# Optimization experiments

Hardware: AMD Instinct MI355X
Metric: run time of the kernel (lower is better)

## Reference

```python
import jax, jax.numpy as jnp
import numpy as np
from jax import lax

LN_EPS = 1e-5

def _expert_ffn_all(x, w1, b1, g_ln, b_ln, w2, b2):
    # x: [B,S,D]; w1: [E,D,F]; w2: [E,F,O]
    h = jnp.einsum('bsd,edf->bsef', x, w1) + b1[None, None]          # [B,S,E,F]
    h = jax.nn.gelu(h, approximate=False)                            # torch default GELU (erf)
    mu = jnp.mean(h, axis=-1, keepdims=True)
    var = jnp.var(h, axis=-1, keepdims=True)
    h = (h - mu) / jnp.sqrt(var + LN_EPS) * g_ln[None, None] + b_ln[None, None]
    return jnp.einsum('bsef,efo->bseo', h, w2) + b2[None, None]      # [B,S,E,O]

def _moe_forward(x, w_gate, w1, b1, g_ln, b_ln, w2, b2):
    B, S, D = x.shape
    E = w_gate.shape[1]
    k = max(1, S // E)  # capacity_factor=1.0
    logits = jnp.einsum('bsd,de->bse', x, w_gate)                    # x_gated [B,S,E]
    probs = jax.nn.softmax(logits, axis=-1)
    # expert-choice top-k along the sequence dim of the raw logits
    _, idx = lax.top_k(jnp.transpose(logits, (0, 2, 1)), k)          # [B,E,k]
    b_ix = jnp.arange(B)[:, None, None]
    e_ix = jnp.arange(E)[None, :, None]
    mask_t = jnp.zeros((B, E, S), dtype=probs.dtype).at[b_ix, e_ix, idx].set(1.0)
    gate_scores = probs * jnp.transpose(mask_t, (0, 2, 1))           # [B,S,E]
    expert_out = _expert_ffn_all(x, w1, b1, g_ln, b_ln, w2, b2)      # [B,S,E,O]
    moe_output = jnp.einsum('bse,bseo->bso', gate_scores, expert_out)
    return moe_output, logits

def setup_inputs() -> dict:
    key = jax.random.key(0)
    ks = jax.random.split(key, 4)
    B, S, D, F, O, E = 2, 2048, 1024, 2048, 1024, 8
    sc1 = 1.0 / np.sqrt(D)
    sc2 = 1.0 / np.sqrt(F)
    return {
        'x': jax.random.normal(ks[0], (B, S, D), jnp.float32),
        'w_gate': jax.random.normal(ks[1], (D, E), jnp.float32) * sc1,
        'w1': jax.random.normal(ks[2], (E, D, F), jnp.float32) * sc1,
        'b1': jnp.zeros((E, F), jnp.float32),
        'g_ln': jnp.ones((E, F), jnp.float32),
        'b_ln': jnp.zeros((E, F), jnp.float32),
        'w2': jax.random.normal(ks[3], (E, F, O), jnp.float32) * sc2,
        'b2': jnp.zeros((E, O), jnp.float32),
    }

def reference(x, w_gate, w1, b1, g_ln, b_ln, w2, b2):
    return _moe_forward(x, w_gate, w1, b1, g_ln, b_ln, w2, b2)
```

## Files before the change

kernel.cpp:

```cpp
#include <hip/hip_runtime.h>
#include <cstdint>
#include <cstddef>

typedef __attribute__((ext_vector_type(8))) short bf16x8;
typedef __attribute__((ext_vector_type(4))) float f32x4;

#define S_    2048
#define D_    1024
#define F_    2048
#define O_    1024
#define E_    8
#define KCAP  256
#define ROWS  512
#define NTOK  4096

#define BM 64
#define BN 64
#define BK 64
#define TILE_ELEMS (BM * BK)

__device__ __forceinline__ unsigned short f2bf(float f) {
  unsigned int u = __float_as_uint(f);
  u = (u + 0x7fffu + ((u >> 16) & 1u)) >> 16;
  return (unsigned short)u;
}
__device__ __forceinline__ float bf2f(unsigned short h) {
  return __uint_as_float(((unsigned int)h) << 16);
}

__device__ __forceinline__ void gload16(void* lds, const void* g) {
  auto gp = (__attribute__((address_space(1))) unsigned int*)(uintptr_t)g;
  auto lp = (__attribute__((address_space(3))) unsigned int*)(unsigned int)(uintptr_t)lds;
  __builtin_amdgcn_global_load_lds(gp, lp, 16, 0, 0);
}

__global__ void gating_kernel(const float* __restrict__ x, const float* __restrict__ wg,
                              float* __restrict__ logits, float* __restrict__ probs,
                              unsigned short* __restrict__ xb) {
  const int wave = threadIdx.x >> 6, lane = threadIdx.x & 63;
  const int t = blockIdx.x * 4 + wave;
  const float* xr = x + (size_t)t * D_;
  double acc[8] = {0, 0, 0, 0, 0, 0, 0, 0};
  const int d0 = lane * 16;
#pragma unroll
  for (int i = 0; i < 4; i++) {
    float4 xv = *(const float4*)&xr[d0 + i * 4];
    union { ushort4 u4; unsigned short u[4]; } cv;
    cv.u[0] = f2bf(xv.x); cv.u[1] = f2bf(xv.y); cv.u[2] = f2bf(xv.z); cv.u[3] = f2bf(xv.w);
    *(ushort4*)&xb[(size_t)t * D_ + d0 + i * 4] = cv.u4;
    float xs[4] = {xv.x, xv.y, xv.z, xv.w};
#pragma unroll
    for (int j = 0; j < 4; j++) {
      const float4* wr = (const float4*)&wg[(size_t)(d0 + i * 4 + j) * 8];
      float4 w0 = wr[0], w1v = wr[1];
      double xd = (double)xs[j];
      acc[0] += xd * (double)w0.x;  acc[1] += xd * (double)w0.y;
      acc[2] += xd * (double)w0.z;  acc[3] += xd * (double)w0.w;
      acc[4] += xd * (double)w1v.x; acc[5] += xd * (double)w1v.y;
      acc[6] += xd * (double)w1v.z; acc[7] += xd * (double)w1v.w;
    }
  }
#pragma unroll
  for (int off = 32; off; off >>= 1) {
#pragma unroll
    for (int e = 0; e < 8; e++) acc[e] += __shfl_down(acc[e], off);
  }
  if (lane == 0) {
    double m = acc[0];
    for (int e = 1; e < 8; e++) m = acc[e] > m ? acc[e] : m;
    double p[8]; double s = 0;
    for (int e = 0; e < 8; e++) { p[e] = exp(acc[e] - m); s += p[e]; }
    const double inv = 1.0 / s;
    for (int e = 0; e < 8; e++) {
      logits[(size_t)t * 8 + e] = (float)acc[e];
      probs [(size_t)t * 8 + e] = (float)(p[e] * inv);
    }
  }
}

__global__ void transpose_cvt_kernel(const float* __restrict__ in, unsigned short* __restrict__ out,
                                     const int R, const int C) {
  __shared__ float t[64][65];
  const int e = blockIdx.z;
  const float* inp = in + (size_t)e * R * C;
  unsigned short* outp = out + (size_t)e * R * C;
  const int r0 = blockIdx.y * 64, c0 = blockIdx.x * 64;
  const int tid = threadIdx.x;
  const int lr = tid >> 4;
  const int lc = (tid & 15) * 4;
#pragma unroll
  for (int i = 0; i < 4; i++) {
    const int r = lr + i * 16;
    const float4 v = *(const float4*)&inp[(size_t)(r0 + r) * C + c0 + lc];
    t[r][lc] = v.x; t[r][lc + 1] = v.y; t[r][lc + 2] = v.z; t[r][lc + 3] = v.w;
  }
  __syncthreads();
#pragma unroll
  for (int i = 0; i < 4; i++) {
    const int oc = lr + i * 16;
    union { ushort4 u4; unsigned short u[4]; } u;
#pragma unroll
    for (int j = 0; j < 4; j++) u.u[j] = f2bf(t[lc + j][oc]);
    *(ushort4*)&outp[(size_t)(c0 + oc) * R + r0 + lc] = u.u4;
  }
}

__global__ void topk_kernel(const float* __restrict__ logits, const float* __restrict__ probs,
                            int* __restrict__ sel, float* __restrict__ gate) {
  __shared__ unsigned int keys[S_];
  const int idx = blockIdx.x;
  const int seg = idx & 7;
  const int be = idx >> 3;
  const int b = be >> 3;
  const int e = be & 7;
  const int tid = threadIdx.x;
  for (int i = tid; i < S_; i += 256) {
    unsigned int u = __float_as_uint(logits[((size_t)(b * S_ + i)) * E_ + e]);
    keys[i] = u ^ ((u & 0x80000000u) ? 0xFFFFFFFFu : 0x80000000u);
  }
  __syncthreads();
  const int s = seg * 256 + tid;
  const unsigned int vk = keys[s];
  const int wave = tid >> 6;
  const int W0 = seg * 256 + wave * 64;
  int rank = 0;
#pragma unroll 4
  for (int i = 0; i < W0; i += 4) {
    const uint4 kv = *(const uint4*)&keys[i];
    rank += (kv.x >= vk) + (kv.y >= vk) + (kv.z >= vk) + (kv.w >= vk);
  }
#pragma unroll
  for (int j = 0; j < 64; j++) {
    const int i = W0 + j;
    const unsigned int kv = keys[i];
    rank += (kv > vk) || (kv == vk && i < s);
  }
#pragma unroll 4
  for (int i = W0 + 64; i < S_; i += 4) {
    const uint4 kv = *(const uint4*)&keys[i];
    rank += (kv.x > vk) + (kv.y > vk) + (kv.z > vk) + (kv.w > vk);
  }
  if (rank < KCAP) {
    sel [e * ROWS + b * KCAP + rank] = b * S_ + s;
    gate[e * ROWS + b * KCAP + rank] = probs[((size_t)(b * S_ + s)) * E_ + e];
  }
}

__global__ __launch_bounds__(256, 4) void gemm1_kernel(
    const unsigned short* __restrict__ xb,
    const unsigned short* __restrict__ w1t,
    const float* __restrict__ b1,
    const int* __restrict__ sel,
    unsigned short* __restrict__ hbuf) {
  __shared__ unsigned short As[2 * TILE_ELEMS];
  __shared__ unsigned short Bs[2 * TILE_ELEMS];
  const int bid = blockIdx.x;
  const int lid = (bid & 7) * 256 + (bid >> 3);
  const int e   = lid >> 8;
  const int rem = lid & 255;
  const int n0  = (rem >> 3) * BN;
  const int m0  = (rem & 7) * BM;
  const int tid = threadIdx.x;
  const int wave = tid >> 6, lane = tid & 63;
  const int wr = wave >> 1, wc = wave & 1;

  const int srow = lane >> 3;
  const int schunk = (lane & 7) ^ srow;
  const unsigned short* asrc[2];
  const unsigned short* bsrc[2];
#pragma unroll
  for (int j = 0; j < 2; j++) {
    const int r = wave * 16 + j * 8 + srow;
    const int tok = sel[e * ROWS + m0 + r];
    asrc[j] = xb + (size_t)tok * D_ + schunk * 8;
    bsrc[j] = w1t + ((size_t)e * F_ + n0 + r) * D_ + schunk * 8;
  }

  f32x4 acc[2][2];
#pragma unroll
  for (int mi = 0; mi < 2; mi++)
#pragma unroll
    for (int nj = 0; nj < 2; nj++) acc[mi][nj] = (f32x4){0.f, 0.f, 0.f, 0.f};

  const int fr = lane & 15;

  auto stage = [&](int buf, int k0) {
#pragma unroll
    for (int j = 0; j < 2; j++) {
      gload16(&As[buf * TILE_ELEMS + (wave * 16 + j * 8) * BK], asrc[j] + k0);
      gload16(&Bs[buf * TILE_ELEMS + (wave * 16 + j * 8) * BK], bsrc[j] + k0);
    }
  };
  auto compute = [&](int buf) {
    const unsigned short* Ab = &As[buf * TILE_ELEMS];
    const unsigned short* Bb = &Bs[buf * TILE_ELEMS];
    bf16x8 a[2][2], b[2][2];
#pragma unroll
    for (int kk = 0; kk < 2; kk++) {
      const int xch = ((kk * 4 + (lane >> 4)) ^ (lane & 7)) * 8;
#pragma unroll
      for (int mi = 0; mi < 2; mi++)
        a[kk][mi] = *(const bf16x8*)&Ab[(wr * 32 + mi * 16 + fr) * BK + xch];
#pragma unroll
      for (int nj = 0; nj < 2; nj++)
        b[kk][nj] = *(const bf16x8*)&Bb[(wc * 32 + nj * 16 + fr) * BK + xch];
    }
#pragma unroll
    for (int kk = 0; kk < 2; kk++)
#pragma unroll
      for (int mi = 0; mi < 2; mi++)
#pragma unroll
        for (int nj = 0; nj < 2; nj++)
          acc[mi][nj] = __builtin_amdgcn_mfma_f32_16x16x32_bf16(a[kk][mi], b[kk][nj], acc[mi][nj], 0, 0, 0);
  };

  stage(0, 0);
  __syncthreads();
  int cur = 0;
  for (int t = 0; t < D_ / BK - 1; t++) {
    stage(cur ^ 1, (t + 1) * BK);
    compute(cur);
    __syncthreads();
    cur ^= 1;
  }
  compute(cur);

  const int lr = (lane >> 4) * 4;
#pragma unroll
  for (int mi = 0; mi < 2; mi++)
#pragma unroll
    for (int nj = 0; nj < 2; nj++)
#pragma unroll
      for (int rg = 0; rg < 4; rg++) {
        const int row = m0 + wr * 32 + mi * 16 + lr + rg;
        const int col = n0 + wc * 32 + nj * 16 + fr;
        float v = acc[mi][nj][rg] + b1[e * F_ + col];
        v = 0.5f * v * (1.0f + erff(v * 0.70710678118654752f));
        hbuf[((size_t)e * ROWS + row) * F_ + col] = f2bf(v);
      }
}

__global__ void ln_kernel(unsigned short* __restrict__ hbuf,
                          const float* __restrict__ g_ln, const float* __restrict__ b_ln) {
  const int row = blockIdx.x;
  const int e = row >> 9;
  unsigned short* hr = hbuf + (size_t)row * F_;
  const int tid = threadIdx.x;
  union { bf16x8 v; unsigned short u[8]; } u;
  u.v = *(const bf16x8*)&hr[tid * 8];
  float vals[8]; float s1 = 0.f, s2 = 0.f;
#pragma unroll
  for (int j = 0; j < 8; j++) { float f = bf2f(u.u[j]); vals[j] = f; s1 += f; s2 += f * f; }
#pragma unroll
  for (int off = 32; off; off >>= 1) { s1 += __shfl_down(s1, off); s2 += __shfl_down(s2, off); }
  __shared__ float rs[8];
  const int wave = tid >> 6, lane = tid & 63;
  if (lane == 0) { rs[wave] = s1; rs[wave + 4] = s2; }
  __syncthreads();
  const float t1 = rs[0] + rs[1] + rs[2] + rs[3];
  const float t2 = rs[4] + rs[5] + rs[6] + rs[7];
  const float mu = t1 * (1.f / F_);
  const float var = t2 * (1.f / F_) - mu * mu;
  const float rstd = rsqrtf(var + 1e-5f);
  const float4* gl4 = (const float4*)(g_ln + (size_t)e * F_ + tid * 8);
  const float4* bl4 = (const float4*)(b_ln + (size_t)e * F_ + tid * 8);
  float4 g0 = gl4[0], g1 = gl4[1], bb0 = bl4[0], bb1 = bl4[1];
  float gs[8] = {g0.x, g0.y, g0.z, g0.w, g1.x, g1.y, g1.z, g1.w};
  float bs[8] = {bb0.x, bb0.y, bb0.z, bb0.w, bb1.x, bb1.y, bb1.z, bb1.w};
  union { bf16x8 v; unsigned short u[8]; } o;
#pragma unroll
  for (int j = 0; j < 8; j++)
    o.u[j] = f2bf((vals[j] - mu) * rstd * gs[j] + bs[j]);
  *(bf16x8*)&hr[tid * 8] = o.v;
}

__global__ __launch_bounds__(256, 4) void gemm2_kernel(
    const unsigned short* __restrict__ hbuf,
    const unsigned short* __restrict__ w2t,
    const float* __restrict__ b2,
    const int* __restrict__ sel, const float* __restrict__ gate,
    float* __restrict__ out) {
  __shared__ unsigned short As[2 * TILE_ELEMS];
  __shared__ unsigned short Bs[2 * TILE_ELEMS];
  const int bid = blockIdx.x;
  const int lid = (bid & 7) * 128 + (bid >> 3);
  const int e   = lid >> 7;
  const int rem = lid & 127;
  const int n0  = (rem >> 3) * BN;
  const int m0  = (rem & 7) * BM;
  const int tid = threadIdx.x;
  const int wave = tid >> 6, lane = tid & 63;
  const int wr = wave >> 1, wc = wave & 1;

  const int srow = lane >> 3;
  const int schunk = (lane & 7) ^ srow;
  const unsigned short* asrc[2];
  const unsigned short* bsrc[2];
#pragma unroll
  for (int j = 0; j < 2; j++) {
    const int r = wave * 16 + j * 8 + srow;
    asrc[j] = hbuf + ((size_t)e * ROWS + m0 + r) * F_ + schunk * 8;
    bsrc[j] = w2t + ((size_t)e * O_ + n0 + r) * F_ + schunk * 8;
  }

  f32x4 acc[2][2];
#pragma unroll
  for (int mi = 0; mi < 2; mi++)
#pragma unroll
    for (int nj = 0; nj < 2; nj++) acc[mi][nj] = (f32x4){0.f, 0.f, 0.f, 0.f};

  const int fr = lane & 15;

  auto stage = [&](int buf, int k0) {
#pragma unroll
    for (int j = 0; j < 2; j++) {
      gload16(&As[buf * TILE_ELEMS + (wave * 16 + j * 8) * BK], asrc[j] + k0);
      gload16(&Bs[buf * TILE_ELEMS + (wave * 16 + j * 8) * BK], bsrc[j] + k0);
    }
  };
  auto compute = [&](int buf) {
    const unsigned short* Ab = &As[buf * TILE_ELEMS];
    const unsigned short* Bb = &Bs[buf * TILE_ELEMS];
    bf16x8 a[2][2], b[2][2];
#pragma unroll
    for (int kk = 0; kk < 2; kk++) {
      const int xch = ((kk * 4 + (lane >> 4)) ^ (lane & 7)) * 8;
#pragma unroll
      for (int mi = 0; mi < 2; mi++)
        a[kk][mi] = *(const bf16x8*)&Ab[(wr * 32 + mi * 16 + fr) * BK + xch];
#pragma unroll
      for (int nj = 0; nj < 2; nj++)
        b[kk][nj] = *(const bf16x8*)&Bb[(wc * 32 + nj * 16 + fr) * BK + xch];
    }
#pragma unroll
    for (int kk = 0; kk < 2; kk++)
#pragma unroll
      for (int mi = 0; mi < 2; mi++)
#pragma unroll
        for (int nj = 0; nj < 2; nj++)
          acc[mi][nj] = __builtin_amdgcn_mfma_f32_16x16x32_bf16(a[kk][mi], b[kk][nj], acc[mi][nj], 0, 0, 0);
  };

  stage(0, 0);
  __syncthreads();
  int cur = 0;
  for (int t = 0; t < F_ / BK - 1; t++) {
    stage(cur ^ 1, (t + 1) * BK);
    compute(cur);
    __syncthreads();
    cur ^= 1;
  }
  compute(cur);

  const int lr = (lane >> 4) * 4;
#pragma unroll
  for (int mi = 0; mi < 2; mi++) {
#pragma unroll
    for (int rg = 0; rg < 4; rg++) {
      const int row = m0 + wr * 32 + mi * 16 + lr + rg;
      const int tok = sel[e * ROWS + row];
      const float g = gate[e * ROWS + row];
#pragma unroll
      for (int nj = 0; nj < 2; nj++) {
        const int col = n0 + wc * 32 + nj * 16 + fr;
        const float v = acc[mi][nj][rg] + b2[e * O_ + col];
        atomicAdd(&out[(size_t)tok * O_ + col], g * v);
      }
    }
  }
}

extern "C" void kernel_launch(void* const* d_in, const int* in_sizes, int n_in,
                              void* d_out, int out_size, void* d_ws, size_t ws_size,
                              hipStream_t stream) {
  const float* x     = (const float*)d_in[0];
  const float* wg    = (const float*)d_in[1];
  const float* w1    = (const float*)d_in[2];
  const float* b1    = (const float*)d_in[3];
  const float* g_ln  = (const float*)d_in[4];
  const float* b_ln  = (const float*)d_in[5];
  const float* w2    = (const float*)d_in[6];
  const float* b2    = (const float*)d_in[7];
  float* out = (float*)d_out;
  float* out_logits = out + (size_t)NTOK * O_;

  char* wsb = (char*)d_ws;
  unsigned short* xb   = (unsigned short*)(wsb + 0);
  unsigned short* w1t  = (unsigned short*)(wsb + 8388608);
  unsigned short* w2t  = (unsigned short*)(wsb + 41943040);
  unsigned short* hbuf = (unsigned short*)(wsb + 75497472);
  float* probs = (float*)(wsb + 92274688);
  int*   sel   = (int*)  (wsb + 92405760);
  float* gate  = (float*)(wsb + 92422144);

  hipMemsetAsync(d_out, 0, (size_t)NTOK * O_ * sizeof(float), stream);

  gating_kernel<<<NTOK / 4, 256, 0, stream>>>(x, wg, out_logits, probs, xb);
  transpose_cvt_kernel<<<dim3(F_ / 64, D_ / 64, E_), 256, 0, stream>>>(w1, w1t, D_, F_);
  transpose_cvt_kernel<<<dim3(O_ / 64, F_ / 64, E_), 256, 0, stream>>>(w2, w2t, F_, O_);
  topk_kernel<<<2 * E_ * 8, 256, 0, stream>>>(out_logits, probs, sel, gate);
  gemm1_kernel<<<(F_ / BN) * (ROWS / BM) * E_, 256, 0, stream>>>(xb, w1t, b1, sel, hbuf);
  ln_kernel<<<E_ * ROWS, 256, 0, stream>>>(hbuf, g_ln, b_ln);
  gemm2_kernel<<<(O_ / BN) * (ROWS / BM) * E_, 256, 0, stream>>>(hbuf, w2t, b2, sel, gate, out);
}
```

Measured before the change: 156.6 us.

## Enlarge GEMM tiles to 128x128 with 8 waves and split-K in gemm2

Both expert GEMMs move from 64x64 tiles with 4 waves to 128x128 tiles with 8 waves, where each wave computes a 64x32 sub-tile. This raises arithmetic intensity per LDS load and cuts redundant global traffic. The pipeline now prefetches two stages ahead using explicit vmcnt waits and raw s_barrier in place of __syncthreads. gemm2 also splits K in half to keep 512 blocks, which doubles the atomic adds into the output and adds the bias only from the first half.

```diff
diff --git a/kernel.cpp b/kernel.cpp
--- a/kernel.cpp
+++ b/kernel.cpp
@@ -14,10 +14,7 @@
 #define ROWS  512
 #define NTOK  4096
 
-#define BM 64
-#define BN 64
 #define BK 64
-#define TILE_ELEMS (BM * BK)
 
 __device__ __forceinline__ unsigned short f2bf(float f) {
   unsigned int u = __float_as_uint(f);
@@ -146,94 +143,95 @@
   }
 }
 
-__global__ __launch_bounds__(256, 4) void gemm1_kernel(
+__global__ __launch_bounds__(512, 4) void gemm1_kernel(
     const unsigned short* __restrict__ xb,
     const unsigned short* __restrict__ w1t,
     const float* __restrict__ b1,
     const int* __restrict__ sel,
     unsigned short* __restrict__ hbuf) {
-  __shared__ unsigned short As[2 * TILE_ELEMS];
-  __shared__ unsigned short Bs[2 * TILE_ELEMS];
+  __shared__ unsigned short As[2][128 * 64];
+  __shared__ unsigned short Bs[2][128 * 64];
   const int bid = blockIdx.x;
-  const int lid = (bid & 7) * 256 + (bid >> 3);
-  const int e   = lid >> 8;
-  const int rem = lid & 255;
-  const int n0  = (rem >> 3) * BN;
-  const int m0  = (rem & 7) * BM;
+  const int lid = (bid & 7) * 64 + (bid >> 3);
+  const int e   = lid >> 6;
+  const int rem = lid & 63;
+  const int m0  = (rem & 3) * 128;
+  const int n0  = (rem >> 2) * 128;
   const int tid = threadIdx.x;
   const int wave = tid >> 6, lane = tid & 63;
-  const int wr = wave >> 1, wc = wave & 1;
-
-  const int srow = lane >> 3;
-  const int schunk = (lane & 7) ^ srow;
-  const unsigned short* asrc[2];
-  const unsigned short* bsrc[2];
-#pragma unroll
-  for (int j = 0; j < 2; j++) {
-    const int r = wave * 16 + j * 8 + srow;
-    const int tok = sel[e * ROWS + m0 + r];
-    asrc[j] = xb + (size_t)tok * D_ + schunk * 8;
-    bsrc[j] = w1t + ((size_t)e * F_ + n0 + r) * D_ + schunk * 8;
-  }
-
-  f32x4 acc[2][2];
-#pragma unroll
-  for (int mi = 0; mi < 2; mi++)
+  const int wrow = wave >> 2;
+  const int wcol = wave & 3;
+
+  const int srow = tid >> 3;
+  const int schunk = ((tid & 7) ^ (srow & 7)) * 8;
+  const unsigned short* a0 = xb + (size_t)sel[e * ROWS + m0 + srow] * D_ + schunk;
+  const unsigned short* a1 = xb + (size_t)sel[e * ROWS + m0 + srow + 64] * D_ + schunk;
+  const unsigned short* b0 = w1t + ((size_t)e * F_ + n0 + srow) * D_ + schunk;
+  const unsigned short* b1p = w1t + ((size_t)e * F_ + n0 + srow + 64) * D_ + schunk;
+  const int ldst0 = wave * 512;
+  const int ldst1 = 4096 + wave * 512;
+
+  f32x4 acc[4][2];
+#pragma unroll
+  for (int mi = 0; mi < 4; mi++)
 #pragma unroll
     for (int nj = 0; nj < 2; nj++) acc[mi][nj] = (f32x4){0.f, 0.f, 0.f, 0.f};
 
+  auto stage = [&](int buf, int t) {
+    const int k0 = t * BK;
+    gload16(&As[buf][ldst0], a0 + k0);
+    gload16(&As[buf][ldst1], a1 + k0);
+    gload16(&Bs[buf][ldst0], b0 + k0);
+    gload16(&Bs[buf][ldst1], b1p + k0);
+  };
   const int fr = lane & 15;
-
-  auto stage = [&](int buf, int k0) {
-#pragma unroll
-    for (int j = 0; j < 2; j++) {
-      gload16(&As[buf * TILE_ELEMS + (wave * 16 + j * 8) * BK], asrc[j] + k0);
-      gload16(&Bs[buf * TILE_ELEMS + (wave * 16 + j * 8) * BK], bsrc[j] + k0);
+  auto compute = [&](int buf) {
+    const unsigned short* Ab = As[buf];
+    const unsigned short* Bb = Bs[buf];
+#pragma unroll
+    for (int kk = 0; kk < 2; kk++) {
+      const int q = kk * 4 + (lane >> 4);
+      bf16x8 a[4], b[2];
+#pragma unroll
+      for (int mi = 0; mi < 4; mi++) {
+        const int r = wrow * 64 + mi * 16 + fr;
+        a[mi] = *(const bf16x8*)&Ab[r * 64 + ((q ^ (r & 7)) * 8)];
+      }
+#pragma unroll
+      for (int nj = 0; nj < 2; nj++) {
+        const int r = wcol * 32 + nj * 16 + fr;
+        b[nj] = *(const bf16x8*)&Bb[r * 64 + ((q ^ (r & 7)) * 8)];
+      }
+#pragma unroll
+      for (int mi = 0; mi < 4; mi++)
+#pragma unroll
+        for (int nj = 0; nj < 2; nj++)
+          acc[mi][nj] = __builtin_amdgcn_mfma_f32_16x16x32_bf16(a[mi], b[nj], acc[mi][nj], 0, 0, 0);
     }
   };
-  auto compute = [&](int buf) {
-    const unsigned short* Ab = &As[buf * TILE_ELEMS];
-    const unsigned short* Bb = &Bs[buf * TILE_ELEMS];
-    bf16x8 a[2][2], b[2][2];
-#pragma unroll
-    for (int kk = 0; kk < 2; kk++) {
-      const int xch = ((kk * 4 + (lane >> 4)) ^ (lane & 7)) * 8;
-#pragma unroll
-      for (int mi = 0; mi < 2; mi++)
-        a[kk][mi] = *(const bf16x8*)&Ab[(wr * 32 + mi * 16 + fr) * BK + xch];
-#pragma unroll
-      for (int nj = 0; nj < 2; nj++)
-        b[kk][nj] = *(const bf16x8*)&Bb[(wc * 32 + nj * 16 + fr) * BK + xch];
-    }
-#pragma unroll
-    for (int kk = 0; kk < 2; kk++)
-#pragma unroll
-      for (int mi = 0; mi < 2; mi++)
-#pragma unroll
-        for (int nj = 0; nj < 2; nj++)
-          acc[mi][nj] = __builtin_amdgcn_mfma_f32_16x16x32_bf16(a[kk][mi], b[kk][nj], acc[mi][nj], 0, 0, 0);
-  };
-
+
+  const int NT = D_ / BK;
   stage(0, 0);
-  __syncthreads();
-  int cur = 0;
-  for (int t = 0; t < D_ / BK - 1; t++) {
-    stage(cur ^ 1, (t + 1) * BK);
-    compute(cur);
-    __syncthreads();
-    cur ^= 1;
-  }
-  compute(cur);
-
-  const int lr = (lane >> 4) * 4;
-#pragma unroll
-  for (int mi = 0; mi < 2; mi++)
+  stage(1, 1);
+  for (int t = 0; t < NT; t++) {
+    if (t < NT - 1) asm volatile("s_waitcnt vmcnt(4)" ::: "memory");
+    else            asm volatile("s_waitcnt vmcnt(0)" ::: "memory");
+    asm volatile("s_barrier" ::: "memory");
+    compute(t & 1);
+    if (t + 2 < NT) {
+      asm volatile("s_barrier" ::: "memory");
+      stage(t & 1, t + 2);
+    }
+  }
+
+#pragma unroll
+  for (int mi = 0; mi < 4; mi++)
 #pragma unroll
     for (int nj = 0; nj < 2; nj++)
 #pragma unroll
       for (int rg = 0; rg < 4; rg++) {
-        const int row = m0 + wr * 32 + mi * 16 + lr + rg;
-        const int col = n0 + wc * 32 + nj * 16 + fr;
+        const int row = m0 + wrow * 64 + mi * 16 + (lane >> 4) * 4 + rg;
+        const int col = n0 + wcol * 32 + nj * 16 + fr;
         float v = acc[mi][nj][rg] + b1[e * F_ + col];
         v = 0.5f * v * (1.0f + erff(v * 0.70710678118654752f));
         hbuf[((size_t)e * ROWS + row) * F_ + col] = f2bf(v);
@@ -274,96 +272,101 @@
   *(bf16x8*)&hr[tid * 8] = o.v;
 }
 
-__global__ __launch_bounds__(256, 4) void gemm2_kernel(
+__global__ __launch_bounds__(512, 4) void gemm2_kernel(
     const unsigned short* __restrict__ hbuf,
     const unsigned short* __restrict__ w2t,
     const float* __restrict__ b2,
     const int* __restrict__ sel, const float* __restrict__ gate,
     float* __restrict__ out) {
-  __shared__ unsigned short As[2 * TILE_ELEMS];
-  __shared__ unsigned short Bs[2 * TILE_ELEMS];
+  __shared__ unsigned short As[2][128 * 64];
+  __shared__ unsigned short Bs[2][128 * 64];
   const int bid = blockIdx.x;
-  const int lid = (bid & 7) * 128 + (bid >> 3);
-  const int e   = lid >> 7;
-  const int rem = lid & 127;
-  const int n0  = (rem >> 3) * BN;
-  const int m0  = (rem & 7) * BM;
+  const int lid = (bid & 7) * 64 + (bid >> 3);
+  const int e   = lid >> 6;
+  const int rem = lid & 63;
+  const int khalf = rem & 1;
+  const int m0  = ((rem >> 1) & 3) * 128;
+  const int n0  = (rem >> 3) * 128;
+  const int koff = khalf * (F_ / 2);
   const int tid = threadIdx.x;
   const int wave = tid >> 6, lane = tid & 63;
-  const int wr = wave >> 1, wc = wave & 1;
-
-  const int srow = lane >> 3;
-  const int schunk = (lane & 7) ^ srow;
-  const unsigned short* asrc[2];
-  const unsigned short* bsrc[2];
-#pragma unroll
-  for (int j = 0; j < 2; j++) {
-    const int r = wave * 16 + j * 8 + srow;
-    asrc[j] = hbuf + ((size_t)e * ROWS + m0 + r) * F_ + schunk * 8;
-    bsrc[j] = w2t + ((size_t)e * O_ + n0 + r) * F_ + schunk * 8;
-  }
-
-  f32x4 acc[2][2];
-#pragma unroll
-  for (int mi = 0; mi < 2; mi++)
+  const int wrow = wave >> 2;
+  const int wcol = wave & 3;
+
+  const int srow = tid >> 3;
+  const int schunk = ((tid & 7) ^ (srow & 7)) * 8;
+  const unsigned short* a0 = hbuf + ((size_t)e * ROWS + m0 + srow) * F_ + koff + schunk;
+  const unsigned short* a1 = hbuf + ((size_t)e * ROWS + m0 + srow + 64) * F_ + koff + schunk;
+  const unsigned short* b0 = w2t + ((size_t)e * O_ + n0 + srow) * F_ + koff + schunk;
+  const unsigned short* b1p = w2t + ((size_t)e * O_ + n0 + srow + 64) * F_ + koff + schunk;
+  const int ldst0 = wave * 512;
+  const int ldst1 = 4096 + wave * 512;
+
+  f32x4 acc[4][2];
+#pragma unroll
+  for (int mi = 0; mi < 4; mi++)
 #pragma unroll
     for (int nj = 0; nj < 2; nj++) acc[mi][nj] = (f32x4){0.f, 0.f, 0.f, 0.f};
 
+  auto stage = [&](int buf, int t) {
+    const int k0 = t * BK;
+    gload16(&As[buf][ldst0], a0 + k0);
+    gload16(&As[buf][ldst1], a1 + k0);
+    gload16(&Bs[buf][ldst0], b0 + k0);
+    gload16(&Bs[buf][ldst1], b1p + k0);
+  };
   const int fr = lane & 15;
-
-  auto stage = [&](int buf, int k0) {
-#pragma unroll
-    for (int j = 0; j < 2; j++) {
-      gload16(&As[buf * TILE_ELEMS + (wave * 16 + j * 8) * BK], asrc[j] + k0);
-      gload16(&Bs[buf * TILE_ELEMS + (wave * 16 + j * 8) * BK], bsrc[j] + k0);
+  auto compute = [&](int buf) {
+    const unsigned short* Ab = As[buf];
+    const unsigned short* Bb = Bs[buf];
+#pragma unroll
+    for (int kk = 0; kk < 2; kk++) {
+      const int q = kk * 4 + (lane >> 4);
+      bf16x8 a[4], b[2];
+#pragma unroll
+      for (int mi = 0; mi < 4; mi++) {
+        const int r = wrow * 64 + mi * 16 + fr;
+        a[mi] = *(const bf16x8*)&Ab[r * 64 + ((q ^ (r & 7)) * 8)];
+      }
+#pragma unroll
+      for (int nj = 0; nj < 2; nj++) {
+        const int r = wcol * 32 + nj * 16 + fr;
+        b[nj] = *(const bf16x8*)&Bb[r * 64 + ((q ^ (r & 7)) * 8)];
+      }
+#pragma unroll
+      for (int mi = 0; mi < 4; mi++)
+#pragma unroll
+        for (int nj = 0; nj < 2; nj++)
+          acc[mi][nj] = __builtin_amdgcn_mfma_f32_16x16x32_bf16(a[mi], b[nj], acc[mi][nj], 0, 0, 0);
     }
   };
-  auto compute = [&](int buf) {
-    const unsigned short* Ab = &As[buf * TILE_ELEMS];
-    const unsigned short* Bb = &Bs[buf * TILE_ELEMS];
-    bf16x8 a[2][2], b[2][2];
-#pragma unroll
-    for (int kk = 0; kk < 2; kk++) {
-      const int xch = ((kk * 4 + (lane >> 4)) ^ (lane & 7)) * 8;
-#pragma unroll
-      for (int mi = 0; mi < 2; mi++)
-        a[kk][mi] = *(const bf16x8*)&Ab[(wr * 32 + mi * 16 + fr) * BK + xch];
-#pragma unroll
-      for (int nj = 0; nj < 2; nj++)
-        b[kk][nj] = *(const bf16x8*)&Bb[(wc * 32 + nj * 16 + fr) * BK + xch];
-    }
-#pragma unroll
-    for (int kk = 0; kk < 2; kk++)
-#pragma unroll
-      for (int mi = 0; mi < 2; mi++)
-#pragma unroll
-        for (int nj = 0; nj < 2; nj++)
-          acc[mi][nj] = __builtin_amdgcn_mfma_f32_16x16x32_bf16(a[kk][mi], b[kk][nj], acc[mi][nj], 0, 0, 0);
-  };
-
+
+  const int NT = (F_ / 2) / BK;
   stage(0, 0);
-  __syncthreads();
-  int cur = 0;
-  for (int t = 0; t < F_ / BK - 1; t++) {
-    stage(cur ^ 1, (t + 1) * BK);
-    compute(cur);
-    __syncthreads();
-    cur ^= 1;
-  }
-  compute(cur);
-
-  const int lr = (lane >> 4) * 4;
-#pragma unroll
-  for (int mi = 0; mi < 2; mi++) {
+  stage(1, 1);
+  for (int t = 0; t < NT; t++) {
+    if (t < NT - 1) asm volatile("s_waitcnt vmcnt(4)" ::: "memory");
+    else            asm volatile("s_waitcnt vmcnt(0)" ::: "memory");
+    asm volatile("s_barrier" ::: "memory");
+    compute(t & 1);
+    if (t + 2 < NT) {
+      asm volatile("s_barrier" ::: "memory");
+      stage(t & 1, t + 2);
+    }
+  }
+
+#pragma unroll
+  for (int mi = 0; mi < 4; mi++) {
 #pragma unroll
     for (int rg = 0; rg < 4; rg++) {
-      const int row = m0 + wr * 32 + mi * 16 + lr + rg;
+      const int row = m0 + wrow * 64 + mi * 16 + (lane >> 4) * 4 + rg;
       const int tok = sel[e * ROWS + row];
       const float g = gate[e * ROWS + row];
 #pragma unroll
       for (int nj = 0; nj < 2; nj++) {
-        const int col = n0 + wc * 32 + nj * 16 + fr;
-        const float v = acc[mi][nj][rg] + b2[e * O_ + col];
+        const int col = n0 + wcol * 32 + nj * 16 + fr;
+        float v = acc[mi][nj][rg];
+        if (khalf == 0) v += b2[e * O_ + col];
         atomicAdd(&out[(size_t)tok * O_ + col], g * v);
       }
     }
@@ -399,7 +402,7 @@
   transpose_cvt_kernel<<<dim3(F_ / 64, D_ / 64, E_), 256, 0, stream>>>(w1, w1t, D_, F_);
   transpose_cvt_kernel<<<dim3(O_ / 64, F_ / 64, E_), 256, 0, stream>>>(w2, w2t, F_, O_);
   topk_kernel<<<2 * E_ * 8, 256, 0, stream>>>(out_logits, probs, sel, gate);
-  gemm1_kernel<<<(F_ / BN) * (ROWS / BM) * E_, 256, 0, stream>>>(xb, w1t, b1, sel, hbuf);
+  gemm1_kernel<<<512, 512, 0, stream>>>(xb, w1t, b1, sel, hbuf);
   ln_kernel<<<E_ * ROWS, 256, 0, stream>>>(hbuf, g_ln, b_ln);
-  gemm2_kernel<<<(O_ / BN) * (ROWS / BM) * E_, 256, 0, stream>>>(hbuf, w2t, b2, sel, gate, out);
-}
+  gemm2_kernel<<<512, 512, 0, stream>>>(hbuf, w2t, b2, sel, gate, out);
+}
```

Measured after the change: 162.7 us. +3.9%, slower.

## Split-K the second GEMM and replace atomic scatter with a per-token combine kernel

Applied to the files above, without the earlier changes.

gemm2 now splits the F reduction into two halves, which doubles the block count, and writes plain partial results to a workspace buffer that reuses the w1t region. A new combine kernel uses a token→row entry map written by topk to sum the gated partials plus bias for each token. This removes the output memset and the float atomics. Both GEMMs also drop LDS double buffering for a single buffer with two barriers per step and raise launch bounds to 8 blocks per CU, which trades load/compute overlap for occupancy.

```diff
diff --git a/kernel.cpp b/kernel.cpp
--- a/kernel.cpp
+++ b/kernel.cpp
@@ -106,7 +106,8 @@
 }
 
 __global__ void topk_kernel(const float* __restrict__ logits, const float* __restrict__ probs,
-                            int* __restrict__ sel, float* __restrict__ gate) {
+                            int* __restrict__ sel, float* __restrict__ gate,
+                            int* __restrict__ entry) {
   __shared__ unsigned int keys[S_];
   const int idx = blockIdx.x;
   const int seg = idx & 7;
@@ -141,19 +142,20 @@
     rank += (kv.x > vk) + (kv.y > vk) + (kv.z > vk) + (kv.w > vk);
   }
   if (rank < KCAP) {
-    sel [e * ROWS + b * KCAP + rank] = b * S_ + s;
-    gate[e * ROWS + b * KCAP + rank] = probs[((size_t)(b * S_ + s)) * E_ + e];
-  }
-}
-
-__global__ __launch_bounds__(256, 4) void gemm1_kernel(
-    const unsigned short* __restrict__ xb,
-    const unsigned short* __restrict__ w1t,
-    const float* __restrict__ b1,
-    const int* __restrict__ sel,
+    const int row = b * KCAP + rank;
+    const int tok = b * S_ + s;
+    sel  [e * ROWS + row] = tok;
+    gate [e * ROWS + row] = probs[(size_t)tok * E_ + e];
+    entry[tok * E_ + e]   = row + 1;
+  }
+}
+
+__global__ __launch_bounds__(256, 8) void gemm1_kernel(
+    const unsigned short* __restrict__ xb, const unsigned short* __restrict__ w1t,
+    const float* __restrict__ b1, const int* __restrict__ sel,
     unsigned short* __restrict__ hbuf) {
-  __shared__ unsigned short As[2 * TILE_ELEMS];
-  __shared__ unsigned short Bs[2 * TILE_ELEMS];
+  __shared__ unsigned short As[TILE_ELEMS];
+  __shared__ unsigned short Bs[TILE_ELEMS];
   const int bid = blockIdx.x;
   const int lid = (bid & 7) * 256 + (bid >> 3);
   const int e   = lid >> 8;
@@ -184,26 +186,24 @@
 
   const int fr = lane & 15;
 
-  auto stage = [&](int buf, int k0) {
+  for (int t = 0; t < D_ / BK; t++) {
+    const int k0 = t * BK;
 #pragma unroll
     for (int j = 0; j < 2; j++) {
-      gload16(&As[buf * TILE_ELEMS + (wave * 16 + j * 8) * BK], asrc[j] + k0);
-      gload16(&Bs[buf * TILE_ELEMS + (wave * 16 + j * 8) * BK], bsrc[j] + k0);
-    }
-  };
-  auto compute = [&](int buf) {
-    const unsigned short* Ab = &As[buf * TILE_ELEMS];
-    const unsigned short* Bb = &Bs[buf * TILE_ELEMS];
+      gload16(&As[(wave * 16 + j * 8) * BK], asrc[j] + k0);
+      gload16(&Bs[(wave * 16 + j * 8) * BK], bsrc[j] + k0);
+    }
+    __syncthreads();
     bf16x8 a[2][2], b[2][2];
 #pragma unroll
     for (int kk = 0; kk < 2; kk++) {
       const int xch = ((kk * 4 + (lane >> 4)) ^ (lane & 7)) * 8;
 #pragma unroll
       for (int mi = 0; mi < 2; mi++)
-        a[kk][mi] = *(const bf16x8*)&Ab[(wr * 32 + mi * 16 + fr) * BK + xch];
+        a[kk][mi] = *(const bf16x8*)&As[(wr * 32 + mi * 16 + fr) * BK + xch];
 #pragma unroll
       for (int nj = 0; nj < 2; nj++)
-        b[kk][nj] = *(const bf16x8*)&Bb[(wc * 32 + nj * 16 + fr) * BK + xch];
+        b[kk][nj] = *(const bf16x8*)&Bs[(wc * 32 + nj * 16 + fr) * BK + xch];
     }
 #pragma unroll
     for (int kk = 0; kk < 2; kk++)
@@ -212,18 +212,8 @@
 #pragma unroll
         for (int nj = 0; nj < 2; nj++)
           acc[mi][nj] = __builtin_amdgcn_mfma_f32_16x16x32_bf16(a[kk][mi], b[kk][nj], acc[mi][nj], 0, 0, 0);
-  };
-
-  stage(0, 0);
-  __syncthreads();
-  int cur = 0;
-  for (int t = 0; t < D_ / BK - 1; t++) {
-    stage(cur ^ 1, (t + 1) * BK);
-    compute(cur);
     __syncthreads();
-    cur ^= 1;
-  }
-  compute(cur);
+  }
 
   const int lr = (lane >> 4) * 4;
 #pragma unroll
@@ -274,20 +264,20 @@
   *(bf16x8*)&hr[tid * 8] = o.v;
 }
 
-__global__ __launch_bounds__(256, 4) void gemm2_kernel(
+__global__ __launch_bounds__(256, 8) void gemm2_partial_kernel(
     const unsigned short* __restrict__ hbuf,
     const unsigned short* __restrict__ w2t,
-    const float* __restrict__ b2,
-    const int* __restrict__ sel, const float* __restrict__ gate,
-    float* __restrict__ out) {
-  __shared__ unsigned short As[2 * TILE_ELEMS];
-  __shared__ unsigned short Bs[2 * TILE_ELEMS];
+    float* __restrict__ part) {
+  __shared__ unsigned short As[TILE_ELEMS];
+  __shared__ unsigned short Bs[TILE_ELEMS];
   const int bid = blockIdx.x;
-  const int lid = (bid & 7) * 128 + (bid >> 3);
-  const int e   = lid >> 7;
-  const int rem = lid & 127;
-  const int n0  = (rem >> 3) * BN;
-  const int m0  = (rem & 7) * BM;
+  const int lid = (bid & 7) * 256 + (bid >> 3);
+  const int e     = lid >> 8;
+  const int rem   = lid & 255;
+  const int khalf = rem & 1;
+  const int m0    = ((rem >> 1) & 7) * BM;
+  const int n0    = (rem >> 4) * BN;
+  const int koff  = khalf * (F_ / 2);
   const int tid = threadIdx.x;
   const int wave = tid >> 6, lane = tid & 63;
   const int wr = wave >> 1, wc = wave & 1;
@@ -299,8 +289,8 @@
 #pragma unroll
   for (int j = 0; j < 2; j++) {
     const int r = wave * 16 + j * 8 + srow;
-    asrc[j] = hbuf + ((size_t)e * ROWS + m0 + r) * F_ + schunk * 8;
-    bsrc[j] = w2t + ((size_t)e * O_ + n0 + r) * F_ + schunk * 8;
+    asrc[j] = hbuf + ((size_t)e * ROWS + m0 + r) * F_ + koff + schunk * 8;
+    bsrc[j] = w2t + ((size_t)e * O_ + n0 + r) * F_ + koff + schunk * 8;
   }
 
   f32x4 acc[2][2];
@@ -311,26 +301,24 @@
 
   const int fr = lane & 15;
 
-  auto stage = [&](int buf, int k0) {
+  for (int t = 0; t < (F_ / 2) / BK; t++) {
+    const int k0 = t * BK;
 #pragma unroll
     for (int j = 0; j < 2; j++) {
-      gload16(&As[buf * TILE_ELEMS + (wave * 16 + j * 8) * BK], asrc[j] + k0);
-      gload16(&Bs[buf * TILE_ELEMS + (wave * 16 + j * 8) * BK], bsrc[j] + k0);
-    }
-  };
-  auto compute = [&](int buf) {
-    const unsigned short* Ab = &As[buf * TILE_ELEMS];
-    const unsigned short* Bb = &Bs[buf * TILE_ELEMS];
+      gload16(&As[(wave * 16 + j * 8) * BK], asrc[j] + k0);
+      gload16(&Bs[(wave * 16 + j * 8) * BK], bsrc[j] + k0);
+    }
+    __syncthreads();
     bf16x8 a[2][2], b[2][2];
 #pragma unroll
     for (int kk = 0; kk < 2; kk++) {
       const int xch = ((kk * 4 + (lane >> 4)) ^ (lane & 7)) * 8;
 #pragma unroll
       for (int mi = 0; mi < 2; mi++)
-        a[kk][mi] = *(const bf16x8*)&Ab[(wr * 32 + mi * 16 + fr) * BK + xch];
+        a[kk][mi] = *(const bf16x8*)&As[(wr * 32 + mi * 16 + fr) * BK + xch];
 #pragma unroll
       for (int nj = 0; nj < 2; nj++)
-        b[kk][nj] = *(const bf16x8*)&Bb[(wc * 32 + nj * 16 + fr) * BK + xch];
+        b[kk][nj] = *(const bf16x8*)&Bs[(wc * 32 + nj * 16 + fr) * BK + xch];
     }
 #pragma unroll
     for (int kk = 0; kk < 2; kk++)
@@ -339,35 +327,46 @@
 #pragma unroll
         for (int nj = 0; nj < 2; nj++)
           acc[mi][nj] = __builtin_amdgcn_mfma_f32_16x16x32_bf16(a[kk][mi], b[kk][nj], acc[mi][nj], 0, 0, 0);
-  };
-
-  stage(0, 0);
-  __syncthreads();
-  int cur = 0;
-  for (int t = 0; t < F_ / BK - 1; t++) {
-    stage(cur ^ 1, (t + 1) * BK);
-    compute(cur);
     __syncthreads();
-    cur ^= 1;
-  }
-  compute(cur);
-
+  }
+
+  float* pbase = part + (size_t)khalf * (E_ * ROWS) * O_;
   const int lr = (lane >> 4) * 4;
 #pragma unroll
-  for (int mi = 0; mi < 2; mi++) {
+  for (int mi = 0; mi < 2; mi++)
 #pragma unroll
     for (int rg = 0; rg < 4; rg++) {
       const int row = m0 + wr * 32 + mi * 16 + lr + rg;
-      const int tok = sel[e * ROWS + row];
-      const float g = gate[e * ROWS + row];
 #pragma unroll
       for (int nj = 0; nj < 2; nj++) {
         const int col = n0 + wc * 32 + nj * 16 + fr;
-        const float v = acc[mi][nj][rg] + b2[e * O_ + col];
-        atomicAdd(&out[(size_t)tok * O_ + col], g * v);
+        pbase[((size_t)(e * ROWS) + row) * O_ + col] = acc[mi][nj][rg];
       }
     }
-  }
+}
+
+__global__ void combine_kernel(const float* __restrict__ part, const int* __restrict__ entry,
+                               const float* __restrict__ gate, const float* __restrict__ b2,
+                               float* __restrict__ out) {
+  const int tok = blockIdx.x;
+  const int c = threadIdx.x * 4;
+  float4 acc = {0.f, 0.f, 0.f, 0.f};
+#pragma unroll
+  for (int e = 0; e < E_; e++) {
+    const int r1 = entry[tok * E_ + e];
+    if (r1) {
+      const int idx = e * ROWS + (r1 - 1);
+      const float g = gate[idx];
+      const float4 p0 = *(const float4*)&part[(size_t)idx * O_ + c];
+      const float4 p1 = *(const float4*)&part[(size_t)(E_ * ROWS + idx) * O_ + c];
+      const float4 bb = *(const float4*)&b2[e * O_ + c];
+      acc.x += g * (p0.x + p1.x + bb.x);
+      acc.y += g * (p0.y + p1.y + bb.y);
+      acc.z += g * (p0.z + p1.z + bb.z);
+      acc.w += g * (p0.w + p1.w + bb.w);
+    }
+  }
+  *(float4*)&out[(size_t)tok * O_ + c] = acc;
 }
 
 extern "C" void kernel_launch(void* const* d_in, const int* in_sizes, int n_in,
@@ -392,14 +391,17 @@
   float* probs = (float*)(wsb + 92274688);
   int*   sel   = (int*)  (wsb + 92405760);
   float* gate  = (float*)(wsb + 92422144);
-
-  hipMemsetAsync(d_out, 0, (size_t)NTOK * O_ * sizeof(float), stream);
+  int*   entry = (int*)  (wsb + 92438528);
+  float* part  = (float*)(wsb + 8388608);
+
+  hipMemsetAsync(entry, 0, (size_t)NTOK * E_ * sizeof(int), stream);
 
   gating_kernel<<<NTOK / 4, 256, 0, stream>>>(x, wg, out_logits, probs, xb);
   transpose_cvt_kernel<<<dim3(F_ / 64, D_ / 64, E_), 256, 0, stream>>>(w1, w1t, D_, F_);
   transpose_cvt_kernel<<<dim3(O_ / 64, F_ / 64, E_), 256, 0, stream>>>(w2, w2t, F_, O_);
-  topk_kernel<<<2 * E_ * 8, 256, 0, stream>>>(out_logits, probs, sel, gate);
+  topk_kernel<<<2 * E_ * 8, 256, 0, stream>>>(out_logits, probs, sel, gate, entry);
   gemm1_kernel<<<(F_ / BN) * (ROWS / BM) * E_, 256, 0, stream>>>(xb, w1t, b1, sel, hbuf);
   ln_kernel<<<E_ * ROWS, 256, 0, stream>>>(hbuf, g_ln, b_ln);
-  gemm2_kernel<<<(O_ / BN) * (ROWS / BM) * E_, 256, 0, stream>>>(hbuf, w2t, b2, sel, gate, out);
-}
+  gemm2_partial_kernel<<<2048, 256, 0, stream>>>(hbuf, w2t, part);
+  combine_kernel<<<NTOK, 256, 0, stream>>>(part, entry, gate, b2, out);
+}
```

Measured after the change: 155.4 us. Within noise of the previous version (-0.8%).
